# Performance work log

Hardware: AMD Instinct MI355X
Metric: run time of the kernel (lower is better)

The kernel has to match this reference:

```python
import jax, jax.numpy as jnp
import numpy as np

N = 8192      # total nodes
B = 8         # graphs in batch
L = 1024      # nodes per graph (max_len)
E = 262144    # edges (before self loops)
IN = 64       # in_channels
H = 8         # heads
C = 32        # hidden_channels (per-head out dim)
D = H * C     # 256, d_model
DFF = 2048    # transformer FFN dim (torch default)
NEG = -1e9


def setup_inputs() -> dict:
    key = jax.random.key(0)
    ks = jax.random.split(key, 24)
    def p(i, shape):
        return jax.random.normal(ks[i], shape, jnp.float32) * 0.02
    x = jax.random.normal(ks[0], (N, IN), jnp.float32)
    src = jax.random.randint(ks[1], (E,), 0, N)
    dst = (src // L) * L + jax.random.randint(ks[2], (E,), 0, L)  # keep edges within a graph
    edge_index = jnp.stack([src, dst]).astype(jnp.int32)
    batch = (jnp.arange(N) // L).astype(jnp.int32)
    return dict(
        x=x, edge_index=edge_index, batch=batch,
        gat_W0=p(3, (D, IN)), gat_W12=p(4, (2, D, D)),
        gat_att_src=p(5, (3, H, C)), gat_att_dst=p(6, (3, H, C)), gat_bias=p(7, (3, D)),
        tf_qkv_w=p(8, (2, 3 * D, D)), tf_qkv_b=p(9, (2, 3 * D)),
        tf_out_w=p(10, (2, D, D)), tf_out_b=p(11, (2, D)),
        tf_ln1_w=jnp.ones((2, D)), tf_ln1_b=jnp.zeros((2, D)),
        tf_ln2_w=jnp.ones((2, D)), tf_ln2_b=jnp.zeros((2, D)),
        tf_ff1_w=p(12, (2, DFF, D)), tf_ff1_b=p(13, (2, DFF)),
        tf_ff2_w=p(14, (2, D, DFF)), tf_ff2_b=p(15, (2, D)),
        pred_w=p(16, (3, D)), pred_b=p(17, (3,)),
    )


def _gat(x, src, dst, W, att_s, att_d, bias):
    # PyG GATConv, concat=True, add_self_loops (appended in caller), eval (no dropout)
    h = (x @ W.T).reshape(-1, H, C)                       # [N,H,C]
    a_s = (h * att_s).sum(-1)                             # [N,H]
    a_d = (h * att_d).sum(-1)
    e = jax.nn.leaky_relu(a_s[src] + a_d[dst], 0.2)       # [E+N,H]
    m = jax.ops.segment_max(e, dst, num_segments=N)       # per-dst softmax
    e = jnp.exp(e - m[dst])
    s = jax.ops.segment_sum(e, dst, num_segments=N)
    alpha = e / s[dst]
    out = jax.ops.segment_sum(h[src] * alpha[..., None], dst, num_segments=N)
    return out.reshape(-1, D) + bias


def _ln(x, w, b):
    mu = x.mean(-1, keepdims=True)
    v = ((x - mu) ** 2).mean(-1, keepdims=True)
    return (x - mu) / jnp.sqrt(v + 1e-5) * w + b


def _tf_layer(x, mask, qkv_w, qkv_b, out_w, out_b, ln1w, ln1b, ln2w, ln2b, f1w, f1b, f2w, f2b):
    # torch TransformerEncoderLayer (post-LN, relu), key padding mask, eval mode
    qkv = x @ qkv_w.T + qkv_b                              # [B,L,3D]
    q, k, v = jnp.split(qkv, 3, -1)
    sh = lambda t: t.reshape(B, L, H, D // H)
    q, k, v = sh(q), sh(k), sh(v)
    sc = jnp.einsum('bqhd,bkhd->bhqk', q, k) * (1.0 / float(np.sqrt(D // H)))
    sc = jnp.where(mask[:, None, None, :], NEG, sc)
    a = jax.nn.softmax(sc, -1)
    o = jnp.einsum('bhqk,bkhd->bqhd', a, v).reshape(B, L, D)
    x = _ln(x + o @ out_w.T + out_b, ln1w, ln1b)
    f = jax.nn.relu(x @ f1w.T + f1b) @ f2w.T + f2b
    return _ln(x + f, ln2w, ln2b)


def reference(x, edge_index, batch, gat_W0, gat_W12, gat_att_src, gat_att_dst, gat_bias,
              tf_qkv_w, tf_qkv_b, tf_out_w, tf_out_b, tf_ln1_w, tf_ln1_b, tf_ln2_w, tf_ln2_b,
              tf_ff1_w, tf_ff1_b, tf_ff2_w, tf_ff2_b, pred_w, pred_b):
    loops = jnp.arange(N, dtype=edge_index.dtype)
    src = jnp.concatenate([edge_index[0], loops])
    dst = jnp.concatenate([edge_index[1], loops])
    h = jax.nn.relu(_gat(x, src, dst, gat_W0, gat_att_src[0], gat_att_dst[0], gat_bias[0]))
    for i in range(2):
        h = jax.nn.relu(_gat(h, src, dst, gat_W12[i], gat_att_src[i + 1], gat_att_dst[i + 1], gat_bias[i + 1]))
    # ragged -> padded [B, L, D] (vectorized scatter instead of python loop)
    seq_lens = jax.ops.segment_sum(jnp.ones(N, jnp.int32), batch, num_segments=B)
    starts = jnp.cumsum(seq_lens) - seq_lens
    pos = jnp.arange(N) - starts[batch]
    xp = jnp.zeros((B, L, D), h.dtype).at[batch, pos].set(h)
    mask = jnp.arange(L)[None, :] >= seq_lens[:, None]     # True = padded key
    for i in range(2):
        xp = _tf_layer(xp, mask, tf_qkv_w[i], tf_qkv_b[i], tf_out_w[i], tf_out_b[i],
                       tf_ln1_w[i], tf_ln1_b[i], tf_ln2_w[i], tf_ln2_b[i],
                       tf_ff1_w[i], tf_ff1_b[i], tf_ff2_w[i], tf_ff2_b[i])
    return xp @ pred_w.T + pred_b                          # [B,L,3]
```

## Files before the change

kernel.cpp:

```cpp
#include <hip/hip_runtime.h>
#include <hip/hip_bf16.h>

#define NN 8192
#define EE 262144
#define BB 8
#define LL 1024
#define HH 8
#define DD 256
#define DFFN 2048

typedef short s8v __attribute__((ext_vector_type(8)));
typedef float f32x4 __attribute__((ext_vector_type(4)));
typedef unsigned short ushort;

__device__ inline ushort f2bf(float f) {
    unsigned u = __float_as_uint(f);
    u = (u + 0x7fffu + ((u >> 16) & 1u)) >> 16;
    return (ushort)u;
}
__device__ inline float bf2f(ushort u) {
    return __uint_as_float(((unsigned)u) << 16);
}

template<bool BIAS, bool RELU, bool RES, bool WF, bool WB>
__global__ __launch_bounds__(256) void mgemm_kernel(
    const ushort* __restrict__ A, const ushort* __restrict__ W,
    const float* __restrict__ bias, const float* __restrict__ res,
    float* __restrict__ Cf, ushort* __restrict__ Cb, int M, int N, int K)
{
    __shared__ ushort As[128 * 64];
    __shared__ ushort Bs[128 * 64];
    int t = threadIdx.x;
    int l = t & 63;
    int quad = l >> 4, l15 = l & 15;
    int r7 = l15 & 7;
    int w = t >> 6;
    int wm = (w >> 1) * 64, wn = (w & 1) * 64;
    int m0 = blockIdx.x * 128, n0 = blockIdx.y * 128;

    f32x4 z = {0.f, 0.f, 0.f, 0.f};
    f32x4 acc[4][4];
#pragma unroll
    for (int i = 0; i < 4; ++i)
#pragma unroll
        for (int j = 0; j < 4; ++j) acc[i][j] = z;

    for (int k0 = 0; k0 < K; k0 += 64) {
#pragma unroll
        for (int i = 0; i < 4; ++i) {
            int chunk = i * 256 + t;
            int r = chunk >> 3, p = chunk & 7;
            int qs = (p ^ (r & 7)) * 8;
            __builtin_amdgcn_global_load_lds(
                (const __attribute__((address_space(1))) unsigned int*)
                    (A + (size_t)(m0 + r) * K + k0 + qs),
                (__attribute__((address_space(3))) unsigned int*)(As + chunk * 8), 16, 0, 0);
            __builtin_amdgcn_global_load_lds(
                (const __attribute__((address_space(1))) unsigned int*)
                    (W + (size_t)(n0 + r) * K + k0 + qs),
                (__attribute__((address_space(3))) unsigned int*)(Bs + chunk * 8), 16, 0, 0);
        }
        __syncthreads();
#pragma unroll
        for (int kk = 0; kk < 2; ++kk) {
            int off = ((kk * 4 + quad) ^ r7) * 8;
            s8v af[4], bfv[4];
#pragma unroll
            for (int i = 0; i < 4; ++i) {
                af[i]  = *(const s8v*)(As + (wm + i * 16 + l15) * 64 + off);
                bfv[i] = *(const s8v*)(Bs + (wn + i * 16 + l15) * 64 + off);
            }
#pragma unroll
            for (int mi = 0; mi < 4; ++mi)
#pragma unroll
                for (int ni = 0; ni < 4; ++ni)
                    acc[mi][ni] = __builtin_amdgcn_mfma_f32_16x16x32_bf16(
                        af[mi], bfv[ni], acc[mi][ni], 0, 0, 0);
        }
        __syncthreads();
    }

#pragma unroll
    for (int mi = 0; mi < 4; ++mi) {
#pragma unroll
        for (int ni = 0; ni < 4; ++ni) {
            int n = n0 + wn + ni * 16 + l15;
#pragma unroll
            for (int r = 0; r < 4; ++r) {
                int m = m0 + wm + mi * 16 + quad * 4 + r;
                float v = acc[mi][ni][r];
                if (BIAS) v += bias[n];
                if (RES)  v += res[(size_t)m * N + n];
                if (RELU) v = fmaxf(v, 0.f);
                if (WF) Cf[(size_t)m * N + n] = v;
                if (WB) Cb[(size_t)m * N + n] = f2bf(v);
            }
        }
    }
}

template<bool ASD>
__global__ __launch_bounds__(256) void mgemm64_kernel(
    const ushort* __restrict__ A, const ushort* __restrict__ W,
    ushort* __restrict__ Cb,
    const float* __restrict__ atts, const float* __restrict__ attd,
    float* __restrict__ a_s, float* __restrict__ a_d, int M, int N, int K)
{
    __shared__ ushort As[64 * 64];
    __shared__ ushort Bs[64 * 64];
    int t = threadIdx.x;
    int l = t & 63;
    int quad = l >> 4, l15 = l & 15;
    int r7 = l15 & 7;
    int w = t >> 6;
    int wm = (w >> 1) * 32, wn = (w & 1) * 32;
    int m0 = blockIdx.x * 64, n0 = blockIdx.y * 64;

    f32x4 z = {0.f, 0.f, 0.f, 0.f};
    f32x4 acc[2][2];
#pragma unroll
    for (int i = 0; i < 2; ++i)
#pragma unroll
        for (int j = 0; j < 2; ++j) acc[i][j] = z;

    for (int k0 = 0; k0 < K; k0 += 64) {
#pragma unroll
        for (int i = 0; i < 2; ++i) {
            int chunk = i * 256 + t;
            int r = chunk >> 3, p = chunk & 7;
            int qs = (p ^ (r & 7)) * 8;
            __builtin_amdgcn_global_load_lds(
                (const __attribute__((address_space(1))) unsigned int*)
                    (A + (size_t)(m0 + r) * K + k0 + qs),
                (__attribute__((address_space(3))) unsigned int*)(As + chunk * 8), 16, 0, 0);
            __builtin_amdgcn_global_load_lds(
                (const __attribute__((address_space(1))) unsigned int*)
                    (W + (size_t)(n0 + r) * K + k0 + qs),
                (__attribute__((address_space(3))) unsigned int*)(Bs + chunk * 8), 16, 0, 0);
        }
        __syncthreads();
#pragma unroll
        for (int kk = 0; kk < 2; ++kk) {
            s8v af[2], bfv[2];
            int off = ((kk * 4 + quad) ^ r7) * 8;
#pragma unroll
            for (int i = 0; i < 2; ++i) {
                af[i]  = *(const s8v*)(As + (wm + i * 16 + l15) * 64 + off);
                bfv[i] = *(const s8v*)(Bs + (wn + i * 16 + l15) * 64 + off);
            }
#pragma unroll
            for (int mi = 0; mi < 2; ++mi)
#pragma unroll
                for (int ni = 0; ni < 2; ++ni)
                    acc[mi][ni] = __builtin_amdgcn_mfma_f32_16x16x32_bf16(
                        af[mi], bfv[ni], acc[mi][ni], 0, 0, 0);
        }
        __syncthreads();
    }

#pragma unroll
    for (int mi = 0; mi < 2; ++mi) {
#pragma unroll
        for (int ni = 0; ni < 2; ++ni) {
            int n = n0 + wn + ni * 16 + l15;
#pragma unroll
            for (int r = 0; r < 4; ++r) {
                int m = m0 + wm + mi * 16 + quad * 4 + r;
                Cb[(size_t)m * N + n] = f2bf(acc[mi][ni][r]);
            }
        }
    }

    if (ASD) {
        int head = ((n0 + wn) >> 5) & 7;
        float as0 = atts[head * 32 + l15];
        float as1 = atts[head * 32 + 16 + l15];
        float ad0 = attd[head * 32 + l15];
        float ad1 = attd[head * 32 + 16 + l15];
#pragma unroll
        for (int mi = 0; mi < 2; ++mi)
#pragma unroll
            for (int r = 0; r < 4; ++r) {
                float sp = acc[mi][0][r] * as0 + acc[mi][1][r] * as1;
                float dp = acc[mi][0][r] * ad0 + acc[mi][1][r] * ad1;
#pragma unroll
                for (int off = 1; off < 16; off <<= 1) {
                    sp += __shfl_xor(sp, off);
                    dp += __shfl_xor(dp, off);
                }
                if (l15 == 0) {
                    int m = m0 + wm + mi * 16 + quad * 4 + r;
                    a_s[m * 8 + head] = sp;
                    a_d[m * 8 + head] = dp;
                }
            }
    }
}

__global__ __launch_bounds__(256) void gemm0_scatter_kernel(
    const ushort* __restrict__ A, const ushort* __restrict__ W,
    ushort* __restrict__ Cb,
    const float* __restrict__ atts, const float* __restrict__ attd,
    float* __restrict__ a_s, float* __restrict__ a_d,
    const int* __restrict__ ei, int* __restrict__ deg, int* __restrict__ col)
{
    __shared__ ushort As[64 * 64];
    __shared__ ushort Bs[64 * 64];
    int t = threadIdx.x;

    if (blockIdx.x >= 512) {
        int e = (blockIdx.x - 512) * 256 + t;
        if (e < EE + NN) {
            int s, d;
            if (e < EE) { s = ei[e]; d = ei[EE + e]; } else { s = e - EE; d = s; }
            int slot = atomicAdd(&deg[d], 1);
            col[(d << 7) + slot] = s;
        }
        return;
    }

    int l = t & 63;
    int quad = l >> 4, l15 = l & 15;
    int r7 = l15 & 7;
    int w = t >> 6;
    int wm = (w >> 1) * 32, wn = (w & 1) * 32;
    int m0 = (blockIdx.x & 127) * 64, n0 = (blockIdx.x >> 7) * 64;
    const int K = 64;

    f32x4 z = {0.f, 0.f, 0.f, 0.f};
    f32x4 acc[2][2];
#pragma unroll
    for (int i = 0; i < 2; ++i)
#pragma unroll
        for (int j = 0; j < 2; ++j) acc[i][j] = z;

#pragma unroll
    for (int i = 0; i < 2; ++i) {
        int chunk = i * 256 + t;
        int r = chunk >> 3, p = chunk & 7;
        int qs = (p ^ (r & 7)) * 8;
        __builtin_amdgcn_global_load_lds(
            (const __attribute__((address_space(1))) unsigned int*)
                (A + (size_t)(m0 + r) * K + qs),
            (__attribute__((address_space(3))) unsigned int*)(As + chunk * 8), 16, 0, 0);
        __builtin_amdgcn_global_load_lds(
            (const __attribute__((address_space(1))) unsigned int*)
                (W + (size_t)(n0 + r) * K + qs),
            (__attribute__((address_space(3))) unsigned int*)(Bs + chunk * 8), 16, 0, 0);
    }
    __syncthreads();
#pragma unroll
    for (int kk = 0; kk < 2; ++kk) {
        s8v af[2], bfv[2];
        int off = ((kk * 4 + quad) ^ r7) * 8;
#pragma unroll
        for (int i = 0; i < 2; ++i) {
            af[i]  = *(const s8v*)(As + (wm + i * 16 + l15) * 64 + off);
            bfv[i] = *(const s8v*)(Bs + (wn + i * 16 + l15) * 64 + off);
        }
#pragma unroll
        for (int mi = 0; mi < 2; ++mi)
#pragma unroll
            for (int ni = 0; ni < 2; ++ni)
                acc[mi][ni] = __builtin_amdgcn_mfma_f32_16x16x32_bf16(
                    af[mi], bfv[ni], acc[mi][ni], 0, 0, 0);
    }

#pragma unroll
    for (int mi = 0; mi < 2; ++mi) {
#pragma unroll
        for (int ni = 0; ni < 2; ++ni) {
            int n = n0 + wn + ni * 16 + l15;
#pragma unroll
            for (int r = 0; r < 4; ++r) {
                int m = m0 + wm + mi * 16 + quad * 4 + r;
                Cb[(size_t)m * DD + n] = f2bf(acc[mi][ni][r]);
            }
        }
    }

    {
        int head = ((n0 + wn) >> 5) & 7;
        float as0 = atts[head * 32 + l15];
        float as1 = atts[head * 32 + 16 + l15];
        float ad0 = attd[head * 32 + l15];
        float ad1 = attd[head * 32 + 16 + l15];
#pragma unroll
        for (int mi = 0; mi < 2; ++mi)
#pragma unroll
            for (int r = 0; r < 4; ++r) {
                float sp = acc[mi][0][r] * as0 + acc[mi][1][r] * as1;
                float dp = acc[mi][0][r] * ad0 + acc[mi][1][r] * ad1;
#pragma unroll
                for (int off = 1; off < 16; off <<= 1) {
                    sp += __shfl_xor(sp, off);
                    dp += __shfl_xor(dp, off);
                }
                if (l15 == 0) {
                    int m = m0 + wm + mi * 16 + quad * 4 + r;
                    a_s[m * 8 + head] = sp;
                    a_d[m * 8 + head] = dp;
                }
            }
    }
}

template<bool PRED>
__global__ __launch_bounds__(256) void mgemm_ln_kernel(
    const ushort* __restrict__ A, const ushort* __restrict__ W,
    const float* __restrict__ bias, const float* __restrict__ res,
    const float* __restrict__ lnw, const float* __restrict__ lnbb,
    float* __restrict__ Xf, ushort* __restrict__ Xb,
    const float* __restrict__ pw, const float* __restrict__ pb,
    float* __restrict__ pout, int M, int K)
{
    __shared__ ushort As[16 * 64];
    __shared__ ushort Bs[256 * 64];
    __shared__ float red[2][4][16];
    __shared__ float predred[4][16][3];

    int t = threadIdx.x;
    int l = t & 63;
    int quad = l >> 4, l15 = l & 15;
    int r7 = l15 & 7;
    int w = t >> 6;
    int m0 = blockIdx.x * 16;
    int n0w = w * 64;

    f32x4 z = {0.f, 0.f, 0.f, 0.f};
    f32x4 acc[4];
#pragma unroll
    for (int i = 0; i < 4; ++i) acc[i] = z;

    for (int k0 = 0; k0 < K; k0 += 64) {
#pragma unroll
        for (int i = 0; i < 8; ++i) {
            int chunk = i * 256 + t;
            int r = chunk >> 3, p = chunk & 7;
            int qs = (p ^ (r & 7)) * 8;
            __builtin_amdgcn_global_load_lds(
                (const __attribute__((address_space(1))) unsigned int*)
                    (W + (size_t)r * K + k0 + qs),
                (__attribute__((address_space(3))) unsigned int*)(Bs + chunk * 8), 16, 0, 0);
        }
        if (t < 128) {
            int r = t >> 3, p = t & 7;
            int qs = (p ^ (r & 7)) * 8;
            __builtin_amdgcn_global_load_lds(
                (const __attribute__((address_space(1))) unsigned int*)
                    (A + (size_t)(m0 + r) * K + k0 + qs),
                (__attribute__((address_space(3))) unsigned int*)(As + t * 8), 16, 0, 0);
        }
        __syncthreads();
#pragma unroll
        for (int kk = 0; kk < 2; ++kk) {
            int off = ((kk * 4 + quad) ^ r7) * 8;
            s8v af = *(const s8v*)(As + l15 * 64 + off);
#pragma unroll
            for (int ni = 0; ni < 4; ++ni) {
                s8v bfv = *(const s8v*)(Bs + (n0w + ni * 16 + l15) * 64 + off);
                acc[ni] = __builtin_amdgcn_mfma_f32_16x16x32_bf16(af, bfv, acc[ni], 0, 0, 0);
            }
        }
        __syncthreads();
    }

    float v[4][4];
#pragma unroll
    for (int ni = 0; ni < 4; ++ni) {
        int n = n0w + ni * 16 + l15;
        float bi = bias[n];
#pragma unroll
        for (int r = 0; r < 4; ++r) {
            int m = m0 + quad * 4 + r;
            v[ni][r] = acc[ni][r] + bi + res[(size_t)m * DD + n];
        }
    }
    float s1[4], s2[4];
#pragma unroll
    for (int r = 0; r < 4; ++r) {
        s1[r] = 0.f; s2[r] = 0.f;
#pragma unroll
        for (int ni = 0; ni < 4; ++ni) { s1[r] += v[ni][r]; s2[r] += v[ni][r] * v[ni][r]; }
#pragma unroll
        for (int off = 1; off < 16; off <<= 1) {
            s1[r] += __shfl_xor(s1[r], off);
            s2[r] += __shfl_xor(s2[r], off);
        }
    }
    if (l15 == 0)
#pragma unroll
        for (int r = 0; r < 4; ++r) {
            red[0][w][quad * 4 + r] = s1[r];
            red[1][w][quad * 4 + r] = s2[r];
        }
    __syncthreads();
    float mu[4], rstd[4];
#pragma unroll
    for (int r = 0; r < 4; ++r) {
        int row = quad * 4 + r;
        float S1 = red[0][0][row] + red[0][1][row] + red[0][2][row] + red[0][3][row];
        float S2 = red[1][0][row] + red[1][1][row] + red[1][2][row] + red[1][3][row];
        mu[r] = S1 * (1.f / 256.f);
        float var = S2 * (1.f / 256.f) - mu[r] * mu[r];
        rstd[r] = rsqrtf(fmaxf(var, 0.f) + 1e-5f);
    }

    float ov[4][4];
#pragma unroll
    for (int ni = 0; ni < 4; ++ni) {
        int n = n0w + ni * 16 + l15;
        float wl = lnw[n], bl = lnbb[n];
#pragma unroll
        for (int r = 0; r < 4; ++r)
            ov[ni][r] = (v[ni][r] - mu[r]) * rstd[r] * wl + bl;
    }

    if (PRED) {
        float ps[3][4] = {};
#pragma unroll
        for (int ni = 0; ni < 4; ++ni) {
            int n = n0w + ni * 16 + l15;
            float w0 = pw[n], w1 = pw[DD + n], w2 = pw[2 * DD + n];
#pragma unroll
            for (int r = 0; r < 4; ++r) {
                ps[0][r] += ov[ni][r] * w0;
                ps[1][r] += ov[ni][r] * w1;
                ps[2][r] += ov[ni][r] * w2;
            }
        }
#pragma unroll
        for (int o3 = 0; o3 < 3; ++o3)
#pragma unroll
            for (int r = 0; r < 4; ++r)
#pragma unroll
                for (int off = 1; off < 16; off <<= 1)
                    ps[o3][r] += __shfl_xor(ps[o3][r], off);
        if (l15 == 0)
#pragma unroll
            for (int o3 = 0; o3 < 3; ++o3)
#pragma unroll
                for (int r = 0; r < 4; ++r)
                    predred[w][quad * 4 + r][o3] = ps[o3][r];
        __syncthreads();
        if (t < 48) {
            int row = t / 3, o3 = t % 3;
            float s = predred[0][row][o3] + predred[1][row][o3]
                    + predred[2][row][o3] + predred[3][row][o3] + pb[o3];
            pout[(size_t)(m0 + row) * 3 + o3] = s;
        }
    } else {
#pragma unroll
        for (int ni = 0; ni < 4; ++ni) {
            int n = n0w + ni * 16 + l15;
#pragma unroll
            for (int r = 0; r < 4; ++r) {
                int m = m0 + quad * 4 + r;
                Xf[(size_t)m * DD + n] = ov[ni][r];
                Xb[(size_t)m * DD + n] = f2bf(ov[ni][r]);
            }
        }
    }
}

__global__ __launch_bounds__(256) void mgemm_qkv_kernel(
    const ushort* __restrict__ A, const ushort* __restrict__ W,
    const float* __restrict__ bias,
    ushort* __restrict__ Qb, ushort* __restrict__ Kb, ushort* __restrict__ Vt,
    int M, int K)
{
    __shared__ ushort As[64 * 64];
    __shared__ ushort Bs[64 * 64];
    int t = threadIdx.x;
    int l = t & 63;
    int quad = l >> 4, l15 = l & 15;
    int r7 = l15 & 7;
    int w = t >> 6;
    int wm = (w >> 1) * 32, wn = (w & 1) * 32;
    int m0 = blockIdx.x * 64, n0 = blockIdx.y * 64;

    f32x4 z = {0.f, 0.f, 0.f, 0.f};
    f32x4 acc[2][2];
#pragma unroll
    for (int i = 0; i < 2; ++i)
#pragma unroll
        for (int j = 0; j < 2; ++j) acc[i][j] = z;

    for (int k0 = 0; k0 < K; k0 += 64) {
#pragma unroll
        for (int i = 0; i < 2; ++i) {
            int chunk = i * 256 + t;
            int r = chunk >> 3, p = chunk & 7;
            int qs = (p ^ (r & 7)) * 8;
            __builtin_amdgcn_global_load_lds(
                (const __attribute__((address_space(1))) unsigned int*)
                    (A + (size_t)(m0 + r) * K + k0 + qs),
                (__attribute__((address_space(3))) unsigned int*)(As + chunk * 8), 16, 0, 0);
            __builtin_amdgcn_global_load_lds(
                (const __attribute__((address_space(1))) unsigned int*)
                    (W + (size_t)(n0 + r) * K + k0 + qs),
                (__attribute__((address_space(3))) unsigned int*)(Bs + chunk * 8), 16, 0, 0);
        }
        __syncthreads();
#pragma unroll
        for (int kk = 0; kk < 2; ++kk) {
            s8v af[2], bfv[2];
            int off = ((kk * 4 + quad) ^ r7) * 8;
#pragma unroll
            for (int i = 0; i < 2; ++i) {
                af[i]  = *(const s8v*)(As + (wm + i * 16 + l15) * 64 + off);
                bfv[i] = *(const s8v*)(Bs + (wn + i * 16 + l15) * 64 + off);
            }
#pragma unroll
            for (int mi = 0; mi < 2; ++mi)
#pragma unroll
                for (int ni = 0; ni < 2; ++ni)
                    acc[mi][ni] = __builtin_amdgcn_mfma_f32_16x16x32_bf16(
                        af[mi], bfv[ni], acc[mi][ni], 0, 0, 0);
        }
        __syncthreads();
    }

#pragma unroll
    for (int mi = 0; mi < 2; ++mi) {
#pragma unroll
        for (int ni = 0; ni < 2; ++ni) {
            int n = n0 + wn + ni * 16 + l15;
            int sec = n >> 8, hc = n & 255;
            int hh = hc >> 5, c = hc & 31;
            float bv = bias[n];
#pragma unroll
            for (int r = 0; r < 4; ++r) {
                int m = m0 + wm + mi * 16 + quad * 4 + r;
                float v = acc[mi][ni][r] + bv;
                int b = m >> 10, ll2 = m & 1023;
                int bh = b * 8 + hh;
                if (sec == 0)
                    Qb[(size_t)bh * 32768 + ll2 * 32 + c] = f2bf(v * 0.17677669529663687f);
                else if (sec == 1)
                    Kb[(size_t)bh * 32768 + ll2 * 32 + c] = f2bf(v);
                else
                    Vt[(size_t)bh * 32768 + c * 1024 + ll2] = f2bf(v);
            }
        }
    }
}

__global__ __launch_bounds__(256) void castall_kernel(
    const float* __restrict__ W0, const float* __restrict__ W12,
    const float* __restrict__ qkvw, const float* __restrict__ outw,
    const float* __restrict__ f1w, const float* __restrict__ f2w,
    const float* __restrict__ x,
    ushort* __restrict__ W0b, ushort* __restrict__ W12b,
    ushort* __restrict__ qkvb, ushort* __restrict__ outb,
    ushort* __restrict__ f1b, ushort* __restrict__ f2b,
    ushort* __restrict__ xb, int* __restrict__ deg)
{
    int tid = blockIdx.x * 256 + threadIdx.x;
    if (tid < 2048) *(int4*)(deg + tid * 4) = make_int4(0, 0, 0, 0);
    int e = tid * 4;
    if (e >= 3293184) return;
    const float* s; ushort* d; int off;
    if (e < 16384)        { s = W0;   d = W0b;  off = e; }
    else if (e < 147456)  { s = W12;  d = W12b; off = e - 16384; }
    else if (e < 540672)  { s = qkvw; d = qkvb; off = e - 147456; }
    else if (e < 671744)  { s = outw; d = outb; off = e - 540672; }
    else if (e < 1720320) { s = f1w;  d = f1b;  off = e - 671744; }
    else if (e < 2768896) { s = f2w;  d = f2b;  off = e - 1720320; }
    else                  { s = x;    d = xb;   off = e - 2768896; }
    float4 v = *(const float4*)(s + off);
    d[off + 0] = f2bf(v.x); d[off + 1] = f2bf(v.y);
    d[off + 2] = f2bf(v.z); d[off + 3] = f2bf(v.w);
}

__global__ __launch_bounds__(256) void gat_agg_kernel(
    const ushort* __restrict__ hlinb, const float* __restrict__ a_s,
    const float* __restrict__ a_d, const int* __restrict__ deg,
    const int* __restrict__ col, const float* __restrict__ bias,
    float* __restrict__ alpha_e,
    float* __restrict__ out, ushort* __restrict__ outb)
{
    int wid = threadIdx.x >> 6, lane = threadIdx.x & 63;
    int dst = blockIdx.x * 4 + wid;
    int start = dst << 7;
    int end = start + deg[dst];
    float ad[HH];
#pragma unroll
    for (int h = 0; h < HH; ++h) ad[h] = a_d[(size_t)dst * HH + h];

    float sm[HH];
#pragma unroll
    for (int h = 0; h < HH; ++h) sm[h] = 0.f;
    for (int e = start + lane; e < end; e += 64) {
        int s = col[e];
        float* al = alpha_e + (size_t)e * HH;
#pragma unroll
        for (int h = 0; h < HH; ++h) {
            float v = a_s[(size_t)s * HH + h] + ad[h];
            v = v > 0.f ? v : 0.2f * v;
            float p = __expf(v);
            sm[h] += p;
            al[h] = p;
        }
    }
#pragma unroll
    for (int h = 0; h < HH; ++h)
#pragma unroll
        for (int off = 32; off; off >>= 1) sm[h] += __shfl_xor(sm[h], off);

    int myh = lane >> 3;
    float invs = 1.f / sm[myh];
    float a0 = 0.f, a1 = 0.f, a2 = 0.f, a3 = 0.f;
    int e = start;
    for (; e + 4 <= end; e += 4) {
        int s0 = col[e], s1 = col[e + 1], s2 = col[e + 2], s3 = col[e + 3];
        float al0 = alpha_e[(size_t)e * HH + myh] * invs;
        float al1 = alpha_e[(size_t)(e + 1) * HH + myh] * invs;
        float al2 = alpha_e[(size_t)(e + 2) * HH + myh] * invs;
        float al3 = alpha_e[(size_t)(e + 3) * HH + myh] * invs;
        uint2 h0 = *(const uint2*)(hlinb + (size_t)s0 * DD + lane * 4);
        uint2 h1 = *(const uint2*)(hlinb + (size_t)s1 * DD + lane * 4);
        uint2 h2 = *(const uint2*)(hlinb + (size_t)s2 * DD + lane * 4);
        uint2 h3 = *(const uint2*)(hlinb + (size_t)s3 * DD + lane * 4);
        a0 += al0 * bf2f((ushort)(h0.x & 0xffff)) + al1 * bf2f((ushort)(h1.x & 0xffff))
            + al2 * bf2f((ushort)(h2.x & 0xffff)) + al3 * bf2f((ushort)(h3.x & 0xffff));
        a1 += al0 * bf2f((ushort)(h0.x >> 16)) + al1 * bf2f((ushort)(h1.x >> 16))
            + al2 * bf2f((ushort)(h2.x >> 16)) + al3 * bf2f((ushort)(h3.x >> 16));
        a2 += al0 * bf2f((ushort)(h0.y & 0xffff)) + al1 * bf2f((ushort)(h1.y & 0xffff))
            + al2 * bf2f((ushort)(h2.y & 0xffff)) + al3 * bf2f((ushort)(h3.y & 0xffff));
        a3 += al0 * bf2f((ushort)(h0.y >> 16)) + al1 * bf2f((ushort)(h1.y >> 16))
            + al2 * bf2f((ushort)(h2.y >> 16)) + al3 * bf2f((ushort)(h3.y >> 16));
    }
    for (; e < end; ++e) {
        int s = col[e];
        float alpha = alpha_e[(size_t)e * HH + myh] * invs;
        uint2 hv = *(const uint2*)(hlinb + (size_t)s * DD + lane * 4);
        a0 += alpha * bf2f((ushort)(hv.x & 0xffff));
        a1 += alpha * bf2f((ushort)(hv.x >> 16));
        a2 += alpha * bf2f((ushort)(hv.y & 0xffff));
        a3 += alpha * bf2f((ushort)(hv.y >> 16));
    }
    float4 bv = *(const float4*)(bias + lane * 4);
    float r0 = fmaxf(a0 + bv.x, 0.f);
    float r1 = fmaxf(a1 + bv.y, 0.f);
    float r2 = fmaxf(a2 + bv.z, 0.f);
    float r3 = fmaxf(a3 + bv.w, 0.f);
    float* op = out + (size_t)dst * DD + lane * 4;
    op[0] = r0; op[1] = r1; op[2] = r2; op[3] = r3;
    ushort* ob = outb + (size_t)dst * DD + lane * 4;
    ob[0] = f2bf(r0); ob[1] = f2bf(r1); ob[2] = f2bf(r2); ob[3] = f2bf(r3);
}

__global__ __launch_bounds__(256, 2) void attn_flash_kernel(
    const ushort* __restrict__ Qb, const ushort* __restrict__ Kb,
    const ushort* __restrict__ Vt, ushort* __restrict__ outb)
{
    __shared__ ushort Ks[2][128 * 32];
    __shared__ ushort Vs[2][32 * 128];
    __shared__ ushort pw[4][32][132];

    int t = threadIdx.x;
    int w = t >> 6, lane = t & 63;
    int quad = lane >> 4, l15 = lane & 15;
    int kq = (quad ^ ((l15 >> 1) & 3)) * 8;
    int bh = blockIdx.y;
    int q0 = blockIdx.x * 128 + w * 32;
    int b = bh >> 3, h = bh & 7;

    const ushort* qbase = Qb + (size_t)bh * 32768;
    const ushort* kbase = Kb + (size_t)bh * 32768;
    const ushort* vbase = Vt + (size_t)bh * 32768;

    s8v aq0 = *(const s8v*)(qbase + (q0 + l15) * 32 + quad * 8);
    s8v aq1 = *(const s8v*)(qbase + (q0 + 16 + l15) * 32 + quad * 8);

    int i0 = t, i1 = 256 + t;
    int kr0 = i0 >> 2, kcs0 = (((i0 & 3)) ^ ((kr0 >> 1) & 3)) * 8;
    int kr1 = i1 >> 2, kcs1 = (((i1 & 3)) ^ ((kr1 >> 1) & 3)) * 8;
    int vr0 = i0 >> 4, vcs0 = ((i0 & 15) ^ (vr0 & 15)) * 8;
    int vr1 = i1 >> 4, vcs1 = ((i1 & 15) ^ (vr1 & 15)) * 8;

#define STAGE(ch, bf)                                                          \
    {                                                                          \
        int j0 = (ch) * 128;                                                   \
        __builtin_amdgcn_global_load_lds(                                      \
            (const __attribute__((address_space(1))) unsigned int*)            \
                (kbase + (size_t)(j0 + kr0) * 32 + kcs0),                      \
            (__attribute__((address_space(3))) unsigned int*)(Ks[bf] + i0 * 8), 16, 0, 0); \
        __builtin_amdgcn_global_load_lds(                                      \
            (const __attribute__((address_space(1))) unsigned int*)            \
                (kbase + (size_t)(j0 + kr1) * 32 + kcs1),                      \
            (__attribute__((address_space(3))) unsigned int*)(Ks[bf] + i1 * 8), 16, 0, 0); \
        __builtin_amdgcn_global_load_lds(                                      \
            (const __attribute__((address_space(1))) unsigned int*)            \
                (vbase + (size_t)vr0 * 1024 + j0 + vcs0),                      \
            (__attribute__((address_space(3))) unsigned int*)(Vs[bf] + i0 * 8), 16, 0, 0); \
        __builtin_amdgcn_global_load_lds(                                      \
            (const __attribute__((address_space(1))) unsigned int*)            \
                (vbase + (size_t)vr1 * 1024 + j0 + vcs1),                      \
            (__attribute__((address_space(3))) unsigned int*)(Vs[bf] + i1 * 8), 16, 0, 0); \
    }

    f32x4 z = {0.f, 0.f, 0.f, 0.f};
    f32x4 o00 = z, o01 = z, o10 = z, o11 = z;
    float lden0[4] = {0.f, 0.f, 0.f, 0.f};
    float lden1[4] = {0.f, 0.f, 0.f, 0.f};

    STAGE(0, 0);
    for (int ch = 0; ch < 8; ++ch) {
        int bf = ch & 1;
        __syncthreads();
        if (ch < 7) STAGE(ch + 1, bf ^ 1);

        f32x4 s0[8], s1[8];
#pragma unroll
        for (int kk = 0; kk < 8; ++kk) {
            s8v bk = *(const s8v*)(Ks[bf] + (kk * 16 + l15) * 32 + kq);
            s0[kk] = __builtin_amdgcn_mfma_f32_16x16x32_bf16(aq0, bk, z, 0, 0, 0);
            s1[kk] = __builtin_amdgcn_mfma_f32_16x16x32_bf16(aq1, bk, z, 0, 0, 0);
        }

        float cs0[4] = {0.f, 0.f, 0.f, 0.f};
        float cs1[4] = {0.f, 0.f, 0.f, 0.f};
#pragma unroll
        for (int kk = 0; kk < 8; ++kk) {
#pragma unroll
            for (int r = 0; r < 4; ++r) {
                float p0 = __expf(s0[kk][r]);
                float p1 = __expf(s1[kk][r]);
                cs0[r] += p0;
                cs1[r] += p1;
                pw[w][quad * 4 + r][kk * 16 + l15]      = f2bf(p0);
                pw[w][16 + quad * 4 + r][kk * 16 + l15] = f2bf(p1);
            }
        }
#pragma unroll
        for (int r = 0; r < 4; ++r) {
#pragma unroll
            for (int off = 1; off < 16; off <<= 1) {
                cs0[r] += __shfl_xor(cs0[r], off);
                cs1[r] += __shfl_xor(cs1[r], off);
            }
            lden0[r] += cs0[r];
            lden1[r] += cs1[r];
        }

#pragma unroll
        for (int kk = 0; kk < 4; ++kk) {
            s8v ap0 = *(const s8v*)(&pw[w][l15][kk * 32 + quad * 8]);
            s8v ap1 = *(const s8v*)(&pw[w][16 + l15][kk * 32 + quad * 8]);
            int c0 = ((kk * 4 + quad) ^ l15) * 8;
            s8v b0 = *(const s8v*)(Vs[bf] + (size_t)l15 * 128 + c0);
            s8v b1 = *(const s8v*)(Vs[bf] + (size_t)(16 + l15) * 128 + c0);
            o00 = __builtin_amdgcn_mfma_f32_16x16x32_bf16(ap0, b0, o00, 0, 0, 0);
            o01 = __builtin_amdgcn_mfma_f32_16x16x32_bf16(ap0, b1, o01, 0, 0, 0);
            o10 = __builtin_amdgcn_mfma_f32_16x16x32_bf16(ap1, b0, o10, 0, 0, 0);
            o11 = __builtin_amdgcn_mfma_f32_16x16x32_bf16(ap1, b1, o11, 0, 0, 0);
        }
    }
#undef STAGE

#pragma unroll
    for (int r = 0; r < 4; ++r) {
        int row0 = q0 + quad * 4 + r;
        int row1 = row0 + 16;
        float i0v = 1.f / lden0[r];
        float i1v = 1.f / lden1[r];
        outb[(size_t)(b * 1024 + row0) * 256 + h * 32 + l15]      = f2bf(o00[r] * i0v);
        outb[(size_t)(b * 1024 + row0) * 256 + h * 32 + 16 + l15] = f2bf(o01[r] * i0v);
        outb[(size_t)(b * 1024 + row1) * 256 + h * 32 + l15]      = f2bf(o10[r] * i1v);
        outb[(size_t)(b * 1024 + row1) * 256 + h * 32 + 16 + l15] = f2bf(o11[r] * i1v);
    }
}

extern "C" void kernel_launch(void* const* d_in, const int* in_sizes, int n_in,
                              void* d_out, int out_size, void* d_ws, size_t ws_size,
                              hipStream_t stream)
{
    const float* x        = (const float*)d_in[0];
    const int*   ei       = (const int*)d_in[1];
    const float* gat_W0   = (const float*)d_in[3];
    const float* gat_W12  = (const float*)d_in[4];
    const float* att_src  = (const float*)d_in[5];
    const float* att_dst  = (const float*)d_in[6];
    const float* gat_bias = (const float*)d_in[7];
    const float* qkv_w    = (const float*)d_in[8];
    const float* qkv_b    = (const float*)d_in[9];
    const float* out_w    = (const float*)d_in[10];
    const float* out_b    = (const float*)d_in[11];
    const float* ln1_w    = (const float*)d_in[12];
    const float* ln1_b    = (const float*)d_in[13];
    const float* ln2_w    = (const float*)d_in[14];
    const float* ln2_b    = (const float*)d_in[15];
    const float* ff1_w    = (const float*)d_in[16];
    const float* ff1_b    = (const float*)d_in[17];
    const float* ff2_w    = (const float*)d_in[18];
    const float* ff2_b    = (const float*)d_in[19];
    const float* pred_w   = (const float*)d_in[20];
    const float* pred_b   = (const float*)d_in[21];
    float* outp = (float*)d_out;

    float* ws   = (float*)d_ws;
    float* hA   = ws;
    float* hB   = ws + 2097152;
    ushort* ffb  = (ushort*)(ws + 4194304);
    ushort* Qb   = (ushort*)(ws + 12582912);
    ushort* Kb   = (ushort*)(ws + 13631488);
    ushort* Vt   = (ushort*)(ws + 14680064);
    ushort* attnb= (ushort*)(ws + 15728640);
    ushort* lnb  = (ushort*)(ws + 16777216);
    ushort* hBb  = (ushort*)(ws + 17825792);
    ushort* xb   = (ushort*)(ws + 18874368);
    ushort* wbase= (ushort*)(ws + 19136512);
    ushort* W0b    = wbase;
    ushort* W12b   = wbase + 16384;
    ushort* qkv_wb = wbase + 147456;
    ushort* out_wb = wbase + 540672;
    ushort* ff1_wb = wbase + 671744;
    ushort* ff2_wb = wbase + 1720320;
    float* a_s  = ws + 20520960;
    float* a_d  = ws + 20586496;
    int*   deg  = (int*)(ws + 20652032);
    ushort* hAb    = (ushort*)(ws + 21000192);
    float*  alpha_e = ws + 22048768;
    int*   col  = (int*)(ws + 30437376);

    castall_kernel<<<3216, 256, 0, stream>>>(
        gat_W0, gat_W12, qkv_w, out_w, ff1_w, ff2_w, x,
        W0b, W12b, qkv_wb, out_wb, ff1_wb, ff2_wb, xb, deg);

    gemm0_scatter_kernel<<<1568, 256, 0, stream>>>(
        xb, W0b, hAb, att_src, att_dst, a_s, a_d, ei, deg, col);
    gat_agg_kernel<<<2048, 256, 0, stream>>>(hAb, a_s, a_d, deg, col, gat_bias,
                                             alpha_e, hB, hBb);

    for (int l = 0; l < 2; ++l) {
        mgemm64_kernel<true><<<dim3(128, 4), 256, 0, stream>>>(
            hBb, W12b + (size_t)l * DD * DD, hAb,
            att_src + (l + 1) * 256, att_dst + (l + 1) * 256, a_s, a_d, NN, DD, DD);
        gat_agg_kernel<<<2048, 256, 0, stream>>>(
            hAb, a_s, a_d, deg, col, gat_bias + (l + 1) * 256, alpha_e, hB, hBb);
    }

    for (int l = 0; l < 2; ++l) {
        mgemm_qkv_kernel<<<dim3(128, 12), 256, 0, stream>>>(
            hBb, qkv_wb + (size_t)l * 768 * DD, qkv_b + l * 768, Qb, Kb, Vt, NN, DD);
        attn_flash_kernel<<<dim3(8, 64), 256, 0, stream>>>(Qb, Kb, Vt, attnb);
        mgemm_ln_kernel<false><<<512, 256, 0, stream>>>(
            attnb, out_wb + (size_t)l * DD * DD, out_b + l * DD, hB,
            ln1_w + l * DD, ln1_b + l * DD, hA, lnb,
            nullptr, nullptr, nullptr, NN, DD);
        mgemm_kernel<true, true, false, false, true><<<dim3(64, 16), 256, 0, stream>>>(
            lnb, ff1_wb + (size_t)l * DFFN * DD, ff1_b + l * DFFN, nullptr,
            nullptr, ffb, NN, DFFN, DD);
        if (l == 0) {
            mgemm_ln_kernel<false><<<512, 256, 0, stream>>>(
                ffb, ff2_wb, ff2_b, hA,
                ln2_w, ln2_b, hB, hBb,
                nullptr, nullptr, nullptr, NN, DFFN);
        } else {
            mgemm_ln_kernel<true><<<512, 256, 0, stream>>>(
                ffb, ff2_wb + (size_t)DD * DFFN, ff2_b + DD, hA,
                ln2_w + DD, ln2_b + DD, nullptr, nullptr,
                pred_w, pred_b, outp, NN, DFFN);
        }
    }
}
```

Before: 393.8 us.

## Fuse GAT softmax into aggregation loop, drop alpha buffer and redundant fp32 writes

The GAT aggregation now computes each edge's exponentiated score inline, per head, during the feature gather. It accumulates the softmax denominator alongside and normalizes once at the end. This removes the separate pass that wrote per-edge alpha values to global memory and read them back. It also skips the fp32 output write for the first two GAT layers, where only the bf16 copy is consumed. In exchange, each lane recomputes the exp for its head, giving 8x redundant exp work per edge across the lanes that share a head.

```diff
diff --git a/kernel.cpp b/kernel.cpp
--- a/kernel.cpp
+++ b/kernel.cpp
@@ -573,80 +573,69 @@
     d[off + 2] = f2bf(v.z); d[off + 3] = f2bf(v.w);
 }
 
+template<bool WF>
 __global__ __launch_bounds__(256) void gat_agg_kernel(
     const ushort* __restrict__ hlinb, const float* __restrict__ a_s,
     const float* __restrict__ a_d, const int* __restrict__ deg,
     const int* __restrict__ col, const float* __restrict__ bias,
-    float* __restrict__ alpha_e,
     float* __restrict__ out, ushort* __restrict__ outb)
 {
     int wid = threadIdx.x >> 6, lane = threadIdx.x & 63;
     int dst = blockIdx.x * 4 + wid;
     int start = dst << 7;
     int end = start + deg[dst];
-    float ad[HH];
-#pragma unroll
-    for (int h = 0; h < HH; ++h) ad[h] = a_d[(size_t)dst * HH + h];
-
-    float sm[HH];
-#pragma unroll
-    for (int h = 0; h < HH; ++h) sm[h] = 0.f;
-    for (int e = start + lane; e < end; e += 64) {
-        int s = col[e];
-        float* al = alpha_e + (size_t)e * HH;
-#pragma unroll
-        for (int h = 0; h < HH; ++h) {
-            float v = a_s[(size_t)s * HH + h] + ad[h];
-            v = v > 0.f ? v : 0.2f * v;
-            float p = __expf(v);
-            sm[h] += p;
-            al[h] = p;
-        }
-    }
-#pragma unroll
-    for (int h = 0; h < HH; ++h)
-#pragma unroll
-        for (int off = 32; off; off >>= 1) sm[h] += __shfl_xor(sm[h], off);
-
     int myh = lane >> 3;
-    float invs = 1.f / sm[myh];
-    float a0 = 0.f, a1 = 0.f, a2 = 0.f, a3 = 0.f;
+    float adh = a_d[(size_t)dst * HH + myh];
+
+    float a0 = 0.f, a1 = 0.f, a2 = 0.f, a3 = 0.f, den = 0.f;
     int e = start;
     for (; e + 4 <= end; e += 4) {
         int s0 = col[e], s1 = col[e + 1], s2 = col[e + 2], s3 = col[e + 3];
-        float al0 = alpha_e[(size_t)e * HH + myh] * invs;
-        float al1 = alpha_e[(size_t)(e + 1) * HH + myh] * invs;
-        float al2 = alpha_e[(size_t)(e + 2) * HH + myh] * invs;
-        float al3 = alpha_e[(size_t)(e + 3) * HH + myh] * invs;
+        float v0 = a_s[(size_t)s0 * HH + myh] + adh;
+        float v1 = a_s[(size_t)s1 * HH + myh] + adh;
+        float v2 = a_s[(size_t)s2 * HH + myh] + adh;
+        float v3 = a_s[(size_t)s3 * HH + myh] + adh;
+        v0 = v0 > 0.f ? v0 : 0.2f * v0;
+        v1 = v1 > 0.f ? v1 : 0.2f * v1;
+        v2 = v2 > 0.f ? v2 : 0.2f * v2;
+        v3 = v3 > 0.f ? v3 : 0.2f * v3;
+        float p0 = __expf(v0), p1 = __expf(v1), p2 = __expf(v2), p3 = __expf(v3);
+        den += p0 + p1 + p2 + p3;
         uint2 h0 = *(const uint2*)(hlinb + (size_t)s0 * DD + lane * 4);
         uint2 h1 = *(const uint2*)(hlinb + (size_t)s1 * DD + lane * 4);
         uint2 h2 = *(const uint2*)(hlinb + (size_t)s2 * DD + lane * 4);
         uint2 h3 = *(const uint2*)(hlinb + (size_t)s3 * DD + lane * 4);
-        a0 += al0 * bf2f((ushort)(h0.x & 0xffff)) + al1 * bf2f((ushort)(h1.x & 0xffff))
-            + al2 * bf2f((ushort)(h2.x & 0xffff)) + al3 * bf2f((ushort)(h3.x & 0xffff));
-        a1 += al0 * bf2f((ushort)(h0.x >> 16)) + al1 * bf2f((ushort)(h1.x >> 16))
-            + al2 * bf2f((ushort)(h2.x >> 16)) + al3 * bf2f((ushort)(h3.x >> 16));
-        a2 += al0 * bf2f((ushort)(h0.y & 0xffff)) + al1 * bf2f((ushort)(h1.y & 0xffff))
-            + al2 * bf2f((ushort)(h2.y & 0xffff)) + al3 * bf2f((ushort)(h3.y & 0xffff));
-        a3 += al0 * bf2f((ushort)(h0.y >> 16)) + al1 * bf2f((ushort)(h1.y >> 16))
-            + al2 * bf2f((ushort)(h2.y >> 16)) + al3 * bf2f((ushort)(h3.y >> 16));
+        a0 += p0 * bf2f((ushort)(h0.x & 0xffff)) + p1 * bf2f((ushort)(h1.x & 0xffff))
+            + p2 * bf2f((ushort)(h2.x & 0xffff)) + p3 * bf2f((ushort)(h3.x & 0xffff));
+        a1 += p0 * bf2f((ushort)(h0.x >> 16)) + p1 * bf2f((ushort)(h1.x >> 16))
+            + p2 * bf2f((ushort)(h2.x >> 16)) + p3 * bf2f((ushort)(h3.x >> 16));
+        a2 += p0 * bf2f((ushort)(h0.y & 0xffff)) + p1 * bf2f((ushort)(h1.y & 0xffff))
+            + p2 * bf2f((ushort)(h2.y & 0xffff)) + p3 * bf2f((ushort)(h3.y & 0xffff));
+        a3 += p0 * bf2f((ushort)(h0.y >> 16)) + p1 * bf2f((ushort)(h1.y >> 16))
+            + p2 * bf2f((ushort)(h2.y >> 16)) + p3 * bf2f((ushort)(h3.y >> 16));
     }
     for (; e < end; ++e) {
         int s = col[e];
-        float alpha = alpha_e[(size_t)e * HH + myh] * invs;
+        float v = a_s[(size_t)s * HH + myh] + adh;
+        v = v > 0.f ? v : 0.2f * v;
+        float p = __expf(v);
+        den += p;
         uint2 hv = *(const uint2*)(hlinb + (size_t)s * DD + lane * 4);
-        a0 += alpha * bf2f((ushort)(hv.x & 0xffff));
-        a1 += alpha * bf2f((ushort)(hv.x >> 16));
-        a2 += alpha * bf2f((ushort)(hv.y & 0xffff));
-        a3 += alpha * bf2f((ushort)(hv.y >> 16));
-    }
+        a0 += p * bf2f((ushort)(hv.x & 0xffff));
+        a1 += p * bf2f((ushort)(hv.x >> 16));
+        a2 += p * bf2f((ushort)(hv.y & 0xffff));
+        a3 += p * bf2f((ushort)(hv.y >> 16));
+    }
+    float inv = 1.f / den;
     float4 bv = *(const float4*)(bias + lane * 4);
-    float r0 = fmaxf(a0 + bv.x, 0.f);
-    float r1 = fmaxf(a1 + bv.y, 0.f);
-    float r2 = fmaxf(a2 + bv.z, 0.f);
-    float r3 = fmaxf(a3 + bv.w, 0.f);
-    float* op = out + (size_t)dst * DD + lane * 4;
-    op[0] = r0; op[1] = r1; op[2] = r2; op[3] = r3;
+    float r0 = fmaxf(a0 * inv + bv.x, 0.f);
+    float r1 = fmaxf(a1 * inv + bv.y, 0.f);
+    float r2 = fmaxf(a2 * inv + bv.z, 0.f);
+    float r3 = fmaxf(a3 * inv + bv.w, 0.f);
+    if (WF) {
+        float* op = out + (size_t)dst * DD + lane * 4;
+        op[0] = r0; op[1] = r1; op[2] = r2; op[3] = r3;
+    }
     ushort* ob = outb + (size_t)dst * DD + lane * 4;
     ob[0] = f2bf(r0); ob[1] = f2bf(r1); ob[2] = f2bf(r2); ob[3] = f2bf(r3);
 }
@@ -822,7 +811,6 @@
     float* a_d  = ws + 20586496;
     int*   deg  = (int*)(ws + 20652032);
     ushort* hAb    = (ushort*)(ws + 21000192);
-    float*  alpha_e = ws + 22048768;
     int*   col  = (int*)(ws + 30437376);
 
     castall_kernel<<<3216, 256, 0, stream>>>(
@@ -831,15 +819,19 @@
 
     gemm0_scatter_kernel<<<1568, 256, 0, stream>>>(
         xb, W0b, hAb, att_src, att_dst, a_s, a_d, ei, deg, col);
-    gat_agg_kernel<<<2048, 256, 0, stream>>>(hAb, a_s, a_d, deg, col, gat_bias,
-                                             alpha_e, hB, hBb);
+    gat_agg_kernel<false><<<2048, 256, 0, stream>>>(
+        hAb, a_s, a_d, deg, col, gat_bias, nullptr, hBb);
 
     for (int l = 0; l < 2; ++l) {
         mgemm64_kernel<true><<<dim3(128, 4), 256, 0, stream>>>(
             hBb, W12b + (size_t)l * DD * DD, hAb,
             att_src + (l + 1) * 256, att_dst + (l + 1) * 256, a_s, a_d, NN, DD, DD);
-        gat_agg_kernel<<<2048, 256, 0, stream>>>(
-            hAb, a_s, a_d, deg, col, gat_bias + (l + 1) * 256, alpha_e, hB, hBb);
+        if (l == 0)
+            gat_agg_kernel<false><<<2048, 256, 0, stream>>>(
+                hAb, a_s, a_d, deg, col, gat_bias + 256, nullptr, hBb);
+        else
+            gat_agg_kernel<true><<<2048, 256, 0, stream>>>(
+                hAb, a_s, a_d, deg, col, gat_bias + 512, hB, hBb);
     }
 
     for (int l = 0; l < 2; ++l) {
```

After: 389.7 us. No clear change (-1.0%).
